# Performance work log

Hardware: AMD Instinct MI355X
Metric: run time of the kernel (lower is better)

The kernel has to match this reference:

```python
import jax, jax.numpy as jnp
import numpy as np
from jax import lax

D_IN, D_OUT = 128, 128
PHI_K, PHIU_K = 100, 100
Q_FACTOR = 1.0
EPS = 1e-8


def _pw_linear(x, knots, coeffs, num_knots):
    """Piecewise-linear eval. Returns (interp, below_mask, above_mask)."""
    in_min, in_max = knots[0], knots[-1]
    xc = jnp.clip(x, in_min, in_max)
    idx = jnp.clip(jnp.searchsorted(knots, xc) - 1, 0, num_knots - 2)
    k0 = knots[idx]
    dk = knots[idx + 1] - k0
    t = jnp.where(dk > EPS, (xc - k0) / dk, jnp.zeros_like(xc))
    interp = (1.0 - t) * coeffs[idx] + t * coeffs[idx + 1]
    return interp, x < in_min, x > in_max


def setup_inputs() -> dict:
    key = jax.random.key(0)
    k1, k2, k3, k4 = jax.random.split(key, 4)
    x = jax.random.uniform(k1, (8192, D_IN), dtype=jnp.float32)  # layer-0 inputs in [0,1]
    phi_log_increments = jnp.full((PHI_K,), np.float32(np.log(1.0 / PHI_K + 1e-6))) \
        + 0.01 * jax.random.normal(k2, (PHI_K,), dtype=jnp.float32)
    Phi_coeffs = jnp.linspace(-10.0, 10.0, PHIU_K, dtype=jnp.float32) \
        + 0.01 * jax.random.normal(k3, (PHIU_K,), dtype=jnp.float32)
    lambdas = jax.random.normal(k4, (D_IN,), dtype=jnp.float32) * np.float32(np.sqrt(2.0 / D_IN))
    eta = jnp.array([1.0 / (D_OUT + 10)], dtype=jnp.float32)
    return {"x": x, "phi_log_increments": phi_log_increments,
            "Phi_coeffs": Phi_coeffs, "lambdas": lambdas, "eta": eta}


def reference(x, phi_log_increments, Phi_coeffs, lambdas, eta):
    eta_s = eta[0]
    q = jnp.arange(D_OUT, dtype=x.dtype)  # [d_out]

    # phi domain (no_grad in torch -> stop_gradient), layer_num == 0
    eta_ng = lax.stop_gradient(eta_s)
    phi_min = jnp.float32(0.0)
    phi_max = 1.0 + eta_ng * (D_OUT - 1)
    phi_knots = phi_min + jnp.arange(PHI_K, dtype=x.dtype) * ((phi_max - phi_min) / (PHI_K - 1))

    # monotonic phi coefficients: normalized cumsum of softplus increments
    inc = jax.nn.softplus(phi_log_increments)
    cum = jnp.cumsum(inc)
    phi_coeffs = cum / (cum[-1] + EPS)

    # shifted inputs: [B, d_in, d_out]
    shifted = x[:, :, None] + eta_s * q[None, None, :]
    interp, below, above = _pw_linear(shifted, phi_knots, phi_coeffs, PHI_K)
    phi_out = jnp.where(below, 0.0, jnp.where(above, 1.0, interp))

    # weighted sum over input dim + q-offset: [B, d_out]
    s = jnp.einsum('bio,i->bo', phi_out, lambdas) + Q_FACTOR * q

    # Phi domain from lambda sums (no_grad)
    lam_ng = lax.stop_gradient(lambdas)
    dmin = jnp.sum(jnp.minimum(lam_ng, 0.0))
    dmax = jnp.sum(jnp.maximum(lam_ng, 0.0)) + Q_FACTOR * (D_OUT - 1)
    Phi_knots = dmin + jnp.arange(PHIU_K, dtype=x.dtype) * ((dmax - dmin) / (PHIU_K - 1))

    interp2, below2, above2 = _pw_linear(s, Phi_knots, Phi_coeffs, PHIU_K)
    left_slope = (Phi_coeffs[1] - Phi_coeffs[0]) / (Phi_knots[1] - Phi_knots[0])
    right_slope = (Phi_coeffs[-1] - Phi_coeffs[-2]) / (Phi_knots[-1] - Phi_knots[-2])
    res = jnp.where(below2, Phi_coeffs[0] + left_slope * (s - dmin), interp2)
    res = jnp.where(above2, Phi_coeffs[-1] + right_slope * (s - dmax), res)
    return res
```

## Files before the change

kernel.cpp:

```cpp
#include <hip/hip_runtime.h>
#include <math.h>

#define D_IN 128
#define D_OUT 128
#define PHI_K 100
#define EPS_F 1e-8f

#define WS_PHI  0
#define WS_PHIU 200
#define WS_SC   400

__global__ void sprecher_setup(const float* __restrict__ phi_log_inc,
                               const float* __restrict__ Phi_coeffs,
                               const float* __restrict__ lambdas,
                               const float* __restrict__ eta,
                               float* __restrict__ ws) {
    __shared__ float sc[128];
    __shared__ float red[2];
    const int t = threadIdx.x;

    float v = 0.0f;
    if (t < PHI_K) {
        float u = phi_log_inc[t];
        v = fmaxf(u, 0.0f) + log1pf(expf(-fabsf(u)));
    }
    sc[t] = v;
    __syncthreads();

    for (int off = 1; off < 128; off <<= 1) {
        float add = (t >= off) ? sc[t - off] : 0.0f;
        __syncthreads();
        sc[t] += add;
        __syncthreads();
    }

    if (t < 64) {
        float a = lambdas[t], b = lambdas[t + 64];
        float smn = fminf(a, 0.0f) + fminf(b, 0.0f);
        float smx = fmaxf(a, 0.0f) + fmaxf(b, 0.0f);
        #pragma unroll
        for (int off = 32; off > 0; off >>= 1) {
            smn += __shfl_down(smn, off, 64);
            smx += __shfl_down(smx, off, 64);
        }
        if (t == 0) { red[0] = smn; red[1] = smx; }
    }
    __syncthreads();

    const float inv_tot = 1.0f / (sc[PHI_K - 1] + EPS_F);

    if (t == 0) {
        float eta_s   = eta[0];
        float phi_max = 1.0f + eta_s * (float)(D_OUT - 1);
        float h1      = phi_max / (float)(PHI_K - 1);

        float dmin  = red[0];
        float dmax  = red[1] + 1.0f * (float)(D_OUT - 1);
        float h2    = (dmax - dmin) / (float)(PHI_K - 1);
        float kmax2 = dmin + (float)(PHI_K - 1) * h2;

        float c0  = Phi_coeffs[0];
        float c1  = Phi_coeffs[1];
        float c98 = Phi_coeffs[PHI_K - 2];
        float c99 = Phi_coeffs[PHI_K - 1];
        float d10  = (dmin + h2) - dmin;
        float kn99 = dmin + (float)(PHI_K - 1) * h2;
        float kn98 = dmin + (float)(PHI_K - 2) * h2;

        ws[WS_SC + 0]  = eta_s;
        ws[WS_SC + 1]  = h1;
        ws[WS_SC + 2]  = 1.0f / h1;
        ws[WS_SC + 4]  = dmin;
        ws[WS_SC + 5]  = h2;
        ws[WS_SC + 6]  = 1.0f / h2;
        ws[WS_SC + 7]  = kmax2;
        ws[WS_SC + 8]  = c0;
        ws[WS_SC + 9]  = c99;
        ws[WS_SC + 10] = (c1 - c0) / d10;
        ws[WS_SC + 11] = (c99 - c98) / (kn99 - kn98);
        ws[WS_SC + 12] = dmax;
    }

    if (t < PHI_K - 1) {
        float ck  = sc[t] * inv_tot;
        float ck1 = sc[t + 1] * inv_tot;
        float d   = ck1 - ck;
        ws[WS_PHI + 2 * t]     = d;
        ws[WS_PHI + 2 * t + 1] = ck - (float)t * d;

        float Ck  = Phi_coeffs[t];
        float Ck1 = Phi_coeffs[t + 1];
        float D   = Ck1 - Ck;
        ws[WS_PHIU + 2 * t]     = D;
        ws[WS_PHIU + 2 * t + 1] = Ck - (float)t * D;
    } else if (t == PHI_K - 1) {
        ws[WS_PHI + 2 * t]      = 0.0f;
        ws[WS_PHI + 2 * t + 1]  = sc[PHI_K - 1] * inv_tot;
        ws[WS_PHIU + 2 * t]     = 0.0f;
        ws[WS_PHIU + 2 * t + 1] = Phi_coeffs[PHI_K - 1];
    }
}

__global__ __launch_bounds__(256) void sprecher_main(
    const float* __restrict__ x,
    const float* __restrict__ lambdas,
    const float* __restrict__ ws,
    float* __restrict__ out) {
    __shared__ float2 phiP[PHI_K];
    __shared__ float2 PhiP[PHI_K];

    const int tid = threadIdx.x;
    const long base = (long)blockIdx.x * 256;

    if (tid < PHI_K) {
        phiP[tid] = reinterpret_cast<const float2*>(ws + WS_PHI)[tid];
    } else if (tid >= 128 && tid < 128 + PHI_K) {
        PhiP[tid - 128] = reinterpret_cast<const float2*>(ws + WS_PHIU)[tid - 128];
    }

    const float eta_s  = ws[WS_SC + 0];
    const float inv_h1 = ws[WS_SC + 2];
    const float dmin   = ws[WS_SC + 4];
    const float inv_h2 = ws[WS_SC + 6];
    const float kmax2  = ws[WS_SC + 7];
    const float c0     = ws[WS_SC + 8];
    const float c99    = ws[WS_SC + 9];
    const float lsl    = ws[WS_SC + 10];
    const float rsl    = ws[WS_SC + 11];
    const float dmax   = ws[WS_SC + 12];

    __syncthreads();

    const int o = tid & (D_OUT - 1);
    const int row = __builtin_amdgcn_readfirstlane(tid >> 7);
    const float* __restrict__ xr = x + base + (long)row * D_IN;

    const float fio = eta_s * (float)o * inv_h1;

    float acc0 = 0.0f, acc1 = 0.0f;

    auto phi1 = [&](float xval, float lam, float& acc) {
        float fi = fmaf(xval, inv_h1, fio);
        int idx = (int)fi;
        float2 cc = phiP[idx];
        acc = fmaf(fmaf(fi, cc.x, cc.y), lam, acc);
    };

    #pragma unroll 8
    for (int i = 0; i < D_IN; i += 4) {
        const float4 xv = *reinterpret_cast<const float4*>(xr + i);
        const float4 lv = *reinterpret_cast<const float4*>(lambdas + i);
        phi1(xv.x, lv.x, acc0);
        phi1(xv.y, lv.y, acc1);
        phi1(xv.z, lv.z, acc0);
        phi1(xv.w, lv.w, acc1);
    }

    float s = acc0 + acc1 + (float)o;

    float xc2 = fminf(fmaxf(s, dmin), kmax2);
    float fi2 = (xc2 - dmin) * inv_h2;
    int idx2 = (int)fi2;
    float2 cc2 = PhiP[idx2];
    float res = fmaf(fi2, cc2.x, cc2.y);
    if (s < dmin)  res = fmaf(lsl, s - dmin, c0);
    if (s > kmax2) res = fmaf(rsl, s - dmax, c99);

    out[base + tid] = res;
}

extern "C" void kernel_launch(void* const* d_in, const int* in_sizes, int n_in,
                              void* d_out, int out_size, void* d_ws, size_t ws_size,
                              hipStream_t stream) {
    const float* x    = (const float*)d_in[0];
    const float* pli  = (const float*)d_in[1];
    const float* Phc  = (const float*)d_in[2];
    const float* lam  = (const float*)d_in[3];
    const float* eta  = (const float*)d_in[4];
    float* ws  = (float*)d_ws;
    float* out = (float*)d_out;

    const int B = in_sizes[0] / D_IN;

    sprecher_setup<<<1, 128, 0, stream>>>(pli, Phc, lam, eta, ws);

    const int total = B * D_OUT;
    sprecher_main<<<total / 256, 256, 0, stream>>>(x, lam, ws, out);
}
```

Measured before the change: 85.03 us.

## Compute three adjacent outputs per thread sharing one paired-segment table lookup

Each thread now evaluates three consecutive output columns (43 threads per row) and stores the phi table as float4 pairs of adjacent segments. Because the per-column offset eta/h1 is below one knot spacing, one LDS lookup serves all three columns, with the next segment chosen by a select. This cuts LDS reads and the redundant x/lambda loads per output. In exchange, the x loads are no longer wave-uniform (rows vary within a wave), output stores become strided and uncoalesced, and the code relies on the column step spanning at most one knot.

Measured after the change: 91.47 us. 1.08x slower.

```diff
diff --git a/kernel.cpp b/kernel.cpp
--- a/kernel.cpp
+++ b/kernel.cpp
@@ -6,9 +6,9 @@
 #define PHI_K 100
 #define EPS_F 1e-8f
 
-#define WS_PHI  0
-#define WS_PHIU 200
-#define WS_SC   400
+#define WS_PHI2 0
+#define WS_PHIU 408
+#define WS_SC   608
 
 __global__ void sprecher_setup(const float* __restrict__ phi_log_inc,
                                const float* __restrict__ Phi_coeffs,
@@ -68,10 +68,8 @@
         float kn98 = dmin + (float)(PHI_K - 2) * h2;
 
         ws[WS_SC + 0]  = eta_s;
-        ws[WS_SC + 1]  = h1;
         ws[WS_SC + 2]  = 1.0f / h1;
         ws[WS_SC + 4]  = dmin;
-        ws[WS_SC + 5]  = h2;
         ws[WS_SC + 6]  = 1.0f / h2;
         ws[WS_SC + 7]  = kmax2;
         ws[WS_SC + 8]  = c0;
@@ -81,21 +79,31 @@
         ws[WS_SC + 12] = dmax;
     }
 
+    auto ab = [&](int k, float& a, float& b) {
+        if (k <= PHI_K - 2) {
+            float ck  = sc[k] * inv_tot;
+            float ck1 = sc[k + 1] * inv_tot;
+            a = ck1 - ck;
+            b = ck - (float)k * a;
+        } else {
+            a = 0.0f;
+            b = sc[PHI_K - 1] * inv_tot;
+        }
+    };
+    if (t < 102) {
+        float a0, b0, a1, b1;
+        ab(t, a0, b0);
+        ab(t + 1, a1, b1);
+        reinterpret_cast<float4*>(ws + WS_PHI2)[t] = make_float4(a0, b0, a1, b1);
+    }
+
     if (t < PHI_K - 1) {
-        float ck  = sc[t] * inv_tot;
-        float ck1 = sc[t + 1] * inv_tot;
-        float d   = ck1 - ck;
-        ws[WS_PHI + 2 * t]     = d;
-        ws[WS_PHI + 2 * t + 1] = ck - (float)t * d;
-
         float Ck  = Phi_coeffs[t];
         float Ck1 = Phi_coeffs[t + 1];
         float D   = Ck1 - Ck;
         ws[WS_PHIU + 2 * t]     = D;
         ws[WS_PHIU + 2 * t + 1] = Ck - (float)t * D;
     } else if (t == PHI_K - 1) {
-        ws[WS_PHI + 2 * t]      = 0.0f;
-        ws[WS_PHI + 2 * t + 1]  = sc[PHI_K - 1] * inv_tot;
         ws[WS_PHIU + 2 * t]     = 0.0f;
         ws[WS_PHIU + 2 * t + 1] = Phi_coeffs[PHI_K - 1];
     }
@@ -105,17 +113,17 @@
     const float* __restrict__ x,
     const float* __restrict__ lambdas,
     const float* __restrict__ ws,
-    float* __restrict__ out) {
-    __shared__ float2 phiP[PHI_K];
-    __shared__ float2 PhiP[PHI_K];
+    float* __restrict__ out,
+    int total_threads) {
+    __shared__ float4 phi2s[102];
+    __shared__ float2 PhiPs[PHI_K];
 
     const int tid = threadIdx.x;
-    const long base = (long)blockIdx.x * 256;
-
-    if (tid < PHI_K) {
-        phiP[tid] = reinterpret_cast<const float2*>(ws + WS_PHI)[tid];
+
+    if (tid < 102) {
+        phi2s[tid] = reinterpret_cast<const float4*>(ws + WS_PHI2)[tid];
     } else if (tid >= 128 && tid < 128 + PHI_K) {
-        PhiP[tid - 128] = reinterpret_cast<const float2*>(ws + WS_PHIU)[tid - 128];
+        PhiPs[tid - 128] = reinterpret_cast<const float2*>(ws + WS_PHIU)[tid - 128];
     }
 
     const float eta_s  = ws[WS_SC + 0];
@@ -131,42 +139,62 @@
 
     __syncthreads();
 
-    const int o = tid & (D_OUT - 1);
-    const int row = __builtin_amdgcn_readfirstlane(tid >> 7);
-    const float* __restrict__ xr = x + base + (long)row * D_IN;
-
-    const float fio = eta_s * (float)o * inv_h1;
-
-    float acc0 = 0.0f, acc1 = 0.0f;
-
-    auto phi1 = [&](float xval, float lam, float& acc) {
-        float fi = fmaf(xval, inv_h1, fio);
-        int idx = (int)fi;
-        float2 cc = phiP[idx];
-        acc = fmaf(fmaf(fi, cc.x, cc.y), lam, acc);
+    const int gid = blockIdx.x * 256 + tid;
+    if (gid >= total_threads) return;
+
+    const int row  = gid / 43;
+    const int slot = gid - row * 43;
+    const int o0   = slot * 3;
+
+    const float* __restrict__ xr = x + (long)row * D_IN;
+
+    const float dfi  = eta_s * inv_h1;
+    const float fio0 = dfi * (float)o0;
+
+    float acc0 = 0.0f, acc1 = 0.0f, acc2 = 0.0f;
+
+    auto eval3 = [&](float xval, float lam) {
+        float fi0 = fmaf(xval, inv_h1, fio0);
+        float fi1 = fi0 + dfi;
+        float fi2 = fi1 + dfi;
+        int idx0 = (int)fi0;
+        float4 cc = phi2s[idx0];
+        acc0 = fmaf(fmaf(fi0, cc.x, cc.y), lam, acc0);
+        int idx1 = (int)fi1;
+        float a1 = (idx1 > idx0) ? cc.z : cc.x;
+        float b1 = (idx1 > idx0) ? cc.w : cc.y;
+        acc1 = fmaf(fmaf(fi1, a1, b1), lam, acc1);
+        int idx2 = (int)fi2;
+        float a2 = (idx2 > idx0) ? cc.z : cc.x;
+        float b2 = (idx2 > idx0) ? cc.w : cc.y;
+        acc2 = fmaf(fmaf(fi2, a2, b2), lam, acc2);
     };
 
     #pragma unroll 8
     for (int i = 0; i < D_IN; i += 4) {
         const float4 xv = *reinterpret_cast<const float4*>(xr + i);
         const float4 lv = *reinterpret_cast<const float4*>(lambdas + i);
-        phi1(xv.x, lv.x, acc0);
-        phi1(xv.y, lv.y, acc1);
-        phi1(xv.z, lv.z, acc0);
-        phi1(xv.w, lv.w, acc1);
-    }
-
-    float s = acc0 + acc1 + (float)o;
-
-    float xc2 = fminf(fmaxf(s, dmin), kmax2);
-    float fi2 = (xc2 - dmin) * inv_h2;
-    int idx2 = (int)fi2;
-    float2 cc2 = PhiP[idx2];
-    float res = fmaf(fi2, cc2.x, cc2.y);
-    if (s < dmin)  res = fmaf(lsl, s - dmin, c0);
-    if (s > kmax2) res = fmaf(rsl, s - dmax, c99);
-
-    out[base + tid] = res;
+        eval3(xv.x, lv.x);
+        eval3(xv.y, lv.y);
+        eval3(xv.z, lv.z);
+        eval3(xv.w, lv.w);
+    }
+
+    float* __restrict__ orow = out + (long)row * D_OUT + o0;
+    #pragma unroll
+    for (int k = 0; k < 3; ++k) {
+        if (o0 + k >= D_OUT) break;
+        float acc = (k == 0) ? acc0 : (k == 1) ? acc1 : acc2;
+        float s = acc + (float)(o0 + k);
+        float xc2 = fminf(fmaxf(s, dmin), kmax2);
+        float fi2 = (xc2 - dmin) * inv_h2;
+        int idx2 = (int)fi2;
+        float2 cc2 = PhiPs[idx2];
+        float res = fmaf(fi2, cc2.x, cc2.y);
+        if (s < dmin)  res = fmaf(lsl, s - dmin, c0);
+        if (s > kmax2) res = fmaf(rsl, s - dmax, c99);
+        orow[k] = res;
+    }
 }
 
 extern "C" void kernel_launch(void* const* d_in, const int* in_sizes, int n_in,
@@ -184,6 +212,7 @@
 
     sprecher_setup<<<1, 128, 0, stream>>>(pli, Phc, lam, eta, ws);
 
-    const int total = B * D_OUT;
-    sprecher_main<<<total / 256, 256, 0, stream>>>(x, lam, ws, out);
+    const int total_threads = B * 43;
+    const int grid = (total_threads + 255) / 256;
+    sprecher_main<<<grid, 256, 0, stream>>>(x, lam, ws, out, total_threads);
 }
```
